# Performance work log

Measured on AMD Instinct MI355X. Metric: run time of the kernel, lower is better.

## Reference

```python
import jax, jax.numpy as jnp
import numpy as np

WH = WW = 7          # window size
N_TOK = WH * WW      # 49 tokens per window
HEADS = 8
HEAD_DIM = 32
DIM = HEADS * HEAD_DIM  # 256
NW = 64              # windows per image (56x56 / 7x7)
BW = 64 * NW         # batch_images * windows = 4096


def _rel_pos_index(wh, ww):
    # Swin-style relative position index, flattened to (N*N,)
    coords = np.stack(np.meshgrid(np.arange(wh), np.arange(ww), indexing='ij'))  # (2, wh, ww)
    coords = coords.reshape(2, -1)                                               # (2, N)
    rel = coords[:, :, None] - coords[:, None, :]                                # (2, N, N)
    rel = rel.transpose(1, 2, 0).astype(np.int64)                                # (N, N, 2)
    rel[:, :, 0] += wh - 1
    rel[:, :, 1] += ww - 1
    rel[:, :, 0] *= 2 * ww - 1
    return jnp.asarray(rel.sum(-1).reshape(-1))                                  # (N*N,)

_REL_IDX = _rel_pos_index(WH, WW)


def setup_inputs() -> dict:
    key = jax.random.key(0)
    ks = jax.random.split(key, 5)
    x = jax.random.normal(ks[0], (BW, N_TOK, DIM), dtype=jnp.float32)
    mask = jnp.zeros((1, NW, 1, N_TOK, N_TOK), dtype=jnp.float32)
    w_qkv = jax.random.normal(ks[1], (DIM, 3 * HEADS * HEAD_DIM), dtype=jnp.float32) * 0.02
    b_qkv = jnp.zeros((3 * HEADS * HEAD_DIM,), dtype=jnp.float32)
    rel_table = jax.random.normal(ks[2], ((2 * WH - 1) * (2 * WW - 1), HEADS), dtype=jnp.float32) * 0.02
    w_out = jax.random.normal(ks[3], (HEADS * HEAD_DIM, DIM), dtype=jnp.float32) * 0.02
    b_out = jnp.zeros((DIM,), dtype=jnp.float32)
    return {"x": x, "mask": mask, "w_qkv": w_qkv, "b_qkv": b_qkv,
            "rel_table": rel_table, "w_out": w_out, "b_out": b_out}


def reference(x, mask, w_qkv, b_qkv, rel_table, w_out, b_out):
    bw, n, d = x.shape
    # QKV projection then split per original Rearrange:
    # 'b n (qkv h hd) -> qkv b h n hd'
    qkv = (x @ w_qkv + b_qkv).reshape(bw, n, 3, HEADS, HEAD_DIM)
    qkv = qkv.transpose(2, 0, 3, 1, 4)  # (3, bw, h, n, hd)
    q, k, v = qkv[0], qkv[1], qkv[2]
    # NOTE: original computes einsum('bnid,bnjd->bnij', k, q): a[i,j] = k_i . q_j
    a = jnp.einsum('bhid,bhjd->bhij', k, q) / jnp.sqrt(jnp.asarray(HEAD_DIM, x.dtype))
    # relative position bias: table gather then '(i j) h -> h i j'
    bias = rel_table[_REL_IDX].reshape(n, n, HEADS).transpose(2, 0, 1)  # (h, n, n)
    a = a + bias
    # mask add: '(b nW) h i j -> b nW h i j', + mask, back
    nw = mask.shape[1]
    a = a.reshape(bw // nw, nw, HEADS, n, n) + mask
    a = a.reshape(bw, HEADS, n, n)
    a = jax.nn.softmax(a, axis=-1)
    y = jnp.einsum('bhij,bhjd->bhid', a, v)        # (bw, h, n, hd)
    y = y.transpose(0, 2, 1, 3).reshape(bw, n, HEADS * HEAD_DIM)
    return y @ w_out + b_out
```

## Files before the change

### kernel.cpp

```cpp
#include <hip/hip_runtime.h>

typedef __attribute__((ext_vector_type(8))) short short8;
typedef __attribute__((ext_vector_type(4))) float f32x4;
typedef unsigned short u16;

#define NTOK 49
#define NBLK 4096
#define LOG2E 1.4426950408889634f

#define XF  0
#define QKP 16384
#define VTF 49152
#define MKF 65536
#define POOLN 73728

#define WS_WQT 0
#define WS_WOT 393216
#define WS_BIAS 524288
#define WS_MKG 655360

__device__ __forceinline__ u16 f2bf(float f) {
  unsigned u = __float_as_uint(f);
  return (u16)((u + 0x7fffu + ((u >> 16) & 1u)) >> 16);
}
__device__ __forceinline__ unsigned packbf(float a, float b) {
  unsigned r;
  asm("v_cvt_pk_bf16_f32 %0, %1, %2" : "=v"(r) : "v"(a), "v"(b));
  return r;
}

__device__ __forceinline__ short8 asm_frag(unsigned c0p0, unsigned c0p1,
                                           unsigned c1p0, unsigned c1p1,
                                           int srcA, int srcB, bool cSel) {
  unsigned a0 = (unsigned)__shfl((int)c0p0, srcA);
  unsigned b0 = (unsigned)__shfl((int)c1p0, srcA);
  unsigned a1 = (unsigned)__shfl((int)c0p1, srcA);
  unsigned b1 = (unsigned)__shfl((int)c1p1, srcA);
  unsigned a2 = (unsigned)__shfl((int)c0p0, srcB);
  unsigned b2 = (unsigned)__shfl((int)c1p0, srcB);
  unsigned a3 = (unsigned)__shfl((int)c0p1, srcB);
  unsigned b3 = (unsigned)__shfl((int)c1p1, srcB);
  union { unsigned u[4]; short8 s8; } r;
  r.u[0] = cSel ? b0 : a0;
  r.u[1] = cSel ? b1 : a1;
  r.u[2] = cSel ? b2 : a2;
  r.u[3] = cSel ? b3 : a3;
  return r.s8;
}

__global__ void prep_kernel(const float* __restrict__ w_qkv,
                            const float* __restrict__ w_out,
                            const float* __restrict__ rel,
                            const float* __restrict__ mask,
                            u16* __restrict__ wqTf,
                            u16* __restrict__ woTf,
                            float* __restrict__ biasf,
                            float* __restrict__ mkg) {
  const int stride = gridDim.x * blockDim.x;
  const int gid = blockIdx.x * blockDim.x + threadIdx.x;
  for (int e = gid; e < 48 * 8 * 64 * 8; e += stride) {
    int eL = e & 7, ln = (e >> 3) & 63, ks = (e >> 9) & 7, ctg = e >> 12;
    int k = ks * 32 + (ln >> 4) * 8 + eL;
    int c = ctg * 16 + (ln & 15);
    wqTf[e] = f2bf(w_qkv[k * 768 + c]);
  }
  for (int e = gid; e < 16 * 8 * 64 * 8; e += stride) {
    int eL = e & 7, ln = (e >> 3) & 63, ks = (e >> 9) & 7, ctg = e >> 12;
    int k = ks * 32 + (ln >> 4) * 8 + eL;
    int c = ctg * 16 + (ln & 15);
    woTf[e] = f2bf(w_out[k * 256 + c]);
  }
  for (int e = gid; e < 8 * 16 * 64 * 4; e += stride) {
    int rg = e & 3, ln = (e >> 2) & 63, t = (e >> 8) & 15, hh = e >> 12;
    int i = (t >> 2) * 16 + (ln & 15);
    int j = (t & 3) * 16 + (ln >> 4) * 4 + rg;
    float v;
    if (j >= NTOK) v = -1e30f;
    else if (i >= NTOK) v = 0.f;
    else {
      int dh = i / 7 - j / 7 + 6;
      int dw = i % 7 - j % 7 + 6;
      v = rel[(dh * 13 + dw) * 8 + hh];
    }
    biasf[e] = v * LOG2E;
  }
  for (int e = gid; e < 64 * 16 * 64 * 4; e += stride) {
    int rg = e & 3, ln = (e >> 2) & 63, t = (e >> 8) & 15, wdw = e >> 12;
    int i = (t >> 2) * 16 + (ln & 15);
    int j = (t & 3) * 16 + (ln >> 4) * 4 + rg;
    mkg[e] = (i < NTOK && j < NTOK) ? mask[wdw * (NTOK * NTOK) + i * NTOK + j] * LOG2E : 0.f;
  }
}

__global__ void __launch_bounds__(1024, 4) winattn_mfma(
    const float* __restrict__ x,
    const float* __restrict__ b_qkv,
    const float* __restrict__ b_out,
    const u16* __restrict__ wqTf,
    const u16* __restrict__ woTf,
    const float* __restrict__ biasf,
    const float* __restrict__ mkg,
    float* __restrict__ out)
{
  __shared__ u16 pool[POOLN];
  const int b = blockIdx.x, tid = threadIdx.x;
  const int lane = tid & 63, lo = lane & 15, hi = lane >> 4;
  const int w = tid >> 6;
  const int h = w & 7;
  const int it0 = (w >> 3) * 2;
  const f32x4 zf = {0.f, 0.f, 0.f, 0.f};
  float* mkf = (float*)(pool + MKF);

  {
    const float4* xg = (const float4*)(x + (size_t)b * (NTOK * 256));
    for (int e = tid; e < 49 * 64; e += 1024) {
      float4 v = xg[e];
      int r = e >> 6, c4 = (e & 63) << 2;
      int addr = (((r >> 4) * 8 + (c4 >> 5)) * 64 + ((c4 >> 3) & 3) * 16 + (r & 15)) * 8 + (c4 & 7);
      *(uint2*)&pool[XF + addr] = make_uint2(packbf(v.x, v.y), packbf(v.z, v.w));
    }
    if (tid < 15 * 64) {
      int e = tid;
      int r = 49 + (e >> 6), c4 = (e & 63) << 2;
      int addr = (((r >> 4) * 8 + (c4 >> 5)) * 64 + ((c4 >> 3) & 3) * 16 + (r & 15)) * 8 + (c4 & 7);
      *(uint2*)&pool[XF + addr] = make_uint2(0u, 0u);
    }
    const float4* mg = (const float4*)(mkg + (size_t)(b & 63) * 4096);
    for (int e = tid; e < 1024; e += 1024) {
      *(float4*)&mkf[e * 4] = mg[e];
    }
  }
  __syncthreads();

  {
    const int ctq0 = 2 * w, ctq1 = 2 * w + 1, ctv = 32 + w;
    f32x4 acc[3][4];
    #pragma unroll
    for (int ct = 0; ct < 3; ++ct)
      #pragma unroll
      for (int rt = 0; rt < 4; ++rt) acc[ct][rt] = zf;
    #pragma unroll
    for (int ks = 0; ks < 8; ++ks) {
      short8 bx[4];
      #pragma unroll
      for (int rt = 0; rt < 4; ++rt)
        bx[rt] = *(const short8*)&pool[XF + ((rt * 8 + ks) * 64 + lane) * 8];
      short8 af0 = *(const short8*)&wqTf[((size_t)(ctq0 * 8 + ks) * 64 + lane) * 8];
      short8 af1 = *(const short8*)&wqTf[((size_t)(ctq1 * 8 + ks) * 64 + lane) * 8];
      short8 afv = *(const short8*)&wqTf[((size_t)(ctv * 8 + ks) * 64 + lane) * 8];
      #pragma unroll
      for (int rt = 0; rt < 4; ++rt) {
        acc[0][rt] = __builtin_amdgcn_mfma_f32_16x16x32_bf16(af0, bx[rt], acc[0][rt], 0, 0, 0);
        acc[1][rt] = __builtin_amdgcn_mfma_f32_16x16x32_bf16(af1, bx[rt], acc[1][rt], 0, 0, 0);
        acc[2][rt] = __builtin_amdgcn_mfma_f32_16x16x32_bf16(bx[rt], afv, acc[2][rt], 0, 0, 0);
      }
    }
    const int qkbase = QKP + (w & 7) * 4096 + ((w >= 8) ? 2048 : 0);
    #pragma unroll
    for (int ct = 0; ct < 2; ++ct) {
      const int ctg = 2 * w + ct;
      f32x4 bias = *(const f32x4*)(b_qkv + ctg * 16 + hi * 4);
      #pragma unroll
      for (int rt = 0; rt < 4; ++rt) {
        f32x4 v = acc[ct][rt] + bias;
        int hi2 = ct * 2 + (hi >> 1);
        int eb = (hi & 1) * 4;
        *(uint2*)&pool[qkbase + (rt * 64 + hi2 * 16 + lo) * 8 + eb] =
            make_uint2(packbf(v[0], v[1]), packbf(v[2], v[3]));
      }
    }
    {
      const int vhead = w >> 1, dblk = w & 1;
      const float bv = b_qkv[ctv * 16 + lo];
      #pragma unroll
      for (int rt = 0; rt < 4; ++rt) {
        f32x4 v = acc[2][rt];
        float v0 = v[0] + bv, v1 = v[1] + bv, v2 = v[2] + bv, v3 = v[3] + bv;
        int f = dblk * 2 + (rt >> 1);
        int hiR = (rt & 1) * 2 + (hi >> 1);
        int eb = (hi & 1) * 4;
        *(uint2*)&pool[VTF + (f * 8 + vhead) * 512 + (hiR * 16 + lo) * 8 + eb] =
            make_uint2(packbf(v0, v1), packbf(v2, v3));
      }
    }
  }
  __syncthreads();

  float rs0 = 0.f, rs1 = 0.f;
  unsigned pkp[4][2][2];
  {
    const float SC = 0.17677669529663687f * LOG2E;
    short8 ka0 = *(const short8*)&pool[QKP + h * 4096 + 2048 + ((it0 + 0) * 64 + lane) * 8];
    short8 ka1 = *(const short8*)&pool[QKP + h * 4096 + 2048 + ((it0 + 1) * 64 + lane) * 8];
    const float* bh = biasf + h * 4096;
    #pragma unroll
    for (int jt = 0; jt < 4; ++jt) {
      short8 qa = *(const short8*)&pool[QKP + h * 4096 + (jt * 64 + lane) * 8];
      f32x4 s0 = __builtin_amdgcn_mfma_f32_16x16x32_bf16(qa, ka0, zf, 0, 0, 0);
      f32x4 s1 = __builtin_amdgcn_mfma_f32_16x16x32_bf16(qa, ka1, zf, 0, 0, 0);
      {
        const int t = (it0 + 0) * 4 + jt;
        f32x4 bm = *(const f32x4*)&bh[(t * 64 + lane) * 4];
        f32x4 mm = *(const f32x4*)&mkf[(t * 64 + lane) * 4];
        float p0 = exp2f(fmaf(s0[0], SC, bm[0] + mm[0]));
        float p1 = exp2f(fmaf(s0[1], SC, bm[1] + mm[1]));
        float p2 = exp2f(fmaf(s0[2], SC, bm[2] + mm[2]));
        float p3 = exp2f(fmaf(s0[3], SC, bm[3] + mm[3]));
        rs0 += (p0 + p1) + (p2 + p3);
        pkp[jt][0][0] = packbf(p0, p1);
        pkp[jt][0][1] = packbf(p2, p3);
      }
      {
        const int t = (it0 + 1) * 4 + jt;
        f32x4 bm = *(const f32x4*)&bh[(t * 64 + lane) * 4];
        f32x4 mm = *(const f32x4*)&mkf[(t * 64 + lane) * 4];
        float p0 = exp2f(fmaf(s1[0], SC, bm[0] + mm[0]));
        float p1 = exp2f(fmaf(s1[1], SC, bm[1] + mm[1]));
        float p2 = exp2f(fmaf(s1[2], SC, bm[2] + mm[2]));
        float p3 = exp2f(fmaf(s1[3], SC, bm[3] + mm[3]));
        rs1 += (p0 + p1) + (p2 + p3);
        pkp[jt][1][0] = packbf(p0, p1);
        pkp[jt][1][1] = packbf(p2, p3);
      }
    }
  }
  float inv0, inv1;
  {
    float r2 = rs0 + __shfl_xor(rs0, 16);
    inv0 = 1.f / (r2 + __shfl_xor(r2, 32));
    float r3 = rs1 + __shfl_xor(rs1, 16);
    inv1 = 1.f / (r3 + __shfl_xor(r3, 32));
  }

  {
    const int srcA = lo + 32 * (hi & 1);
    const int srcB = srcA + 16;
    const bool cSel = (hi & 2) != 0;
    short8 va[2][2];
    #pragma unroll
    for (int dblk = 0; dblk < 2; ++dblk)
      #pragma unroll
      for (int k2 = 0; k2 < 2; ++k2)
        va[dblk][k2] = *(const short8*)&pool[VTF + ((dblk * 2 + k2) * 8 + h) * 512 + lane * 8];
    f32x4 ya[2][2];
    ya[0][0] = zf; ya[0][1] = zf; ya[1][0] = zf; ya[1][1] = zf;
    #pragma unroll
    for (int itL = 0; itL < 2; ++itL)
      #pragma unroll
      for (int k2 = 0; k2 < 2; ++k2) {
        short8 pb = asm_frag(pkp[2 * k2][itL][0], pkp[2 * k2][itL][1],
                             pkp[2 * k2 + 1][itL][0], pkp[2 * k2 + 1][itL][1], srcA, srcB, cSel);
        ya[0][itL] = __builtin_amdgcn_mfma_f32_16x16x32_bf16(va[0][k2], pb, ya[0][itL], 0, 0, 0);
        ya[1][itL] = __builtin_amdgcn_mfma_f32_16x16x32_bf16(va[1][k2], pb, ya[1][itL], 0, 0, 0);
      }
    #pragma unroll
    for (int itL = 0; itL < 2; ++itL) {
      const float iv = itL ? inv1 : inv0;
      #pragma unroll
      for (int dblk = 0; dblk < 2; ++dblk) {
        f32x4 yy = ya[dblk][itL];
        int hi2 = dblk * 2 + (hi >> 1);
        int eb = (hi & 1) * 4;
        *(uint2*)&pool[XF + (((it0 + itL) * 8 + h) * 64 + hi2 * 16 + lo) * 8 + eb] =
            make_uint2(packbf(yy[0] * iv, yy[1] * iv), packbf(yy[2] * iv, yy[3] * iv));
      }
    }
  }
  __syncthreads();

  {
    f32x4 pacc[4];
    pacc[0] = zf; pacc[1] = zf; pacc[2] = zf; pacc[3] = zf;
    #pragma unroll
    for (int ks = 0; ks < 8; ++ks) {
      short8 wf = *(const short8*)&woTf[((size_t)(w * 8 + ks) * 64 + lane) * 8];
      #pragma unroll
      for (int rt = 0; rt < 4; ++rt) {
        short8 yb = *(const short8*)&pool[XF + ((rt * 8 + ks) * 64 + lane) * 8];
        pacc[rt] = __builtin_amdgcn_mfma_f32_16x16x32_bf16(wf, yb, pacc[rt], 0, 0, 0);
      }
    }
    float* og = out + (size_t)b * (NTOK * 256);
    const int cb = w * 16 + hi * 4;
    f32x4 bb = *(const f32x4*)(b_out + cb);
    #pragma unroll
    for (int rt = 0; rt < 4; ++rt) {
      const int r = rt * 16 + lo;
      if (r < NTOK) {
        f32x4 vv = pacc[rt] + bb;
        *(f32x4*)(og + (size_t)r * 256 + cb) = vv;
      }
    }
  }
}

extern "C" void kernel_launch(void* const* d_in, const int* in_sizes, int n_in,
                              void* d_out, int out_size, void* d_ws, size_t ws_size,
                              hipStream_t stream) {
  const float *x = nullptr, *mask = nullptr, *w_qkv = nullptr, *b_qkv = nullptr,
              *rel_t = nullptr, *w_out = nullptr, *b_out = nullptr;
  for (int i = 0; i < n_in; ++i) {
    const float* p = (const float*)d_in[i];
    switch (in_sizes[i]) {
      case 4096 * 49 * 256: x = p; break;
      case 64 * 49 * 49:    mask = p; break;
      case 256 * 768:       w_qkv = p; break;
      case 768:             b_qkv = p; break;
      case 169 * 8:         rel_t = p; break;
      case 256 * 256:       w_out = p; break;
      case 256:             b_out = p; break;
    }
  }
  char* wsb = (char*)d_ws;
  u16* wqTf    = (u16*)(wsb + WS_WQT);
  u16* woTf    = (u16*)(wsb + WS_WOT);
  float* biasf = (float*)(wsb + WS_BIAS);
  float* mkg   = (float*)(wsb + WS_MKG);

  hipLaunchKernelGGL(prep_kernel, dim3(1024), dim3(256), 0, stream,
                     w_qkv, w_out, rel_t, mask, wqTf, woTf, biasf, mkg);
  hipLaunchKernelGGL(winattn_mfma, dim3(NBLK), dim3(1024), 0, stream,
                     x, b_qkv, b_out, wqTf, woTf, biasf, mkg, (float*)d_out);
}
```

Before: 301.7 us.

## Fold softmax scale into Q weights and precombine bias+mask table

Pre-scales the Q columns of the QKV weight and bias by the softmax scale times log2e, which removes a multiply from the score path. A new prep kernel builds a combined per-window, per-head bias+mask table (8 MB) in the workspace, so the main kernel reads one global table instead of staging the mask in shared memory. This shrinks LDS use and removes the mask load and the sync work that went with it. The trade is a larger global read footprint per block and an extra prep launch, with a fallback to the old path when the workspace is too small.

```diff
diff --git a/kernel.cpp b/kernel.cpp
--- a/kernel.cpp
+++ b/kernel.cpp
@@ -11,13 +11,15 @@
 #define XF  0
 #define QKP 16384
 #define VTF 49152
-#define MKF 65536
-#define POOLN 73728
+#define POOLN 65536
 
 #define WS_WQT 0
 #define WS_WOT 393216
-#define WS_BIAS 524288
-#define WS_MKG 655360
+#define WS_BQS 524288
+#define WS_BIAS 528384
+#define WS_MKG 659456
+#define WS_CMB 1708032
+#define WS_NEED (WS_CMB + 8388608)
 
 __device__ __forceinline__ u16 f2bf(float f) {
   unsigned u = __float_as_uint(f);
@@ -52,17 +54,22 @@
                             const float* __restrict__ w_out,
                             const float* __restrict__ rel,
                             const float* __restrict__ mask,
+                            const float* __restrict__ b_qkv,
                             u16* __restrict__ wqTf,
                             u16* __restrict__ woTf,
+                            float* __restrict__ bqs,
                             float* __restrict__ biasf,
                             float* __restrict__ mkg) {
+  const float SCQ = 0.17677669529663687f * LOG2E;
   const int stride = gridDim.x * blockDim.x;
   const int gid = blockIdx.x * blockDim.x + threadIdx.x;
   for (int e = gid; e < 48 * 8 * 64 * 8; e += stride) {
     int eL = e & 7, ln = (e >> 3) & 63, ks = (e >> 9) & 7, ctg = e >> 12;
     int k = ks * 32 + (ln >> 4) * 8 + eL;
     int c = ctg * 16 + (ln & 15);
-    wqTf[e] = f2bf(w_qkv[k * 768 + c]);
+    float wv = w_qkv[k * 768 + c];
+    if (ctg < 16) wv *= SCQ;
+    wqTf[e] = f2bf(wv);
   }
   for (int e = gid; e < 16 * 8 * 64 * 8; e += stride) {
     int eL = e & 7, ln = (e >> 3) & 63, ks = (e >> 9) & 7, ctg = e >> 12;
@@ -70,6 +77,8 @@
     int c = ctg * 16 + (ln & 15);
     woTf[e] = f2bf(w_out[k * 256 + c]);
   }
+  for (int e = gid; e < 768; e += stride)
+    bqs[e] = b_qkv[e] * (e < 256 ? SCQ : 1.f);
   for (int e = gid; e < 8 * 16 * 64 * 4; e += stride) {
     int rg = e & 3, ln = (e >> 2) & 63, t = (e >> 8) & 15, hh = e >> 12;
     int i = (t >> 2) * 16 + (ln & 15);
@@ -92,14 +101,25 @@
   }
 }
 
+__global__ void prep2_kernel(const float* __restrict__ biasf,
+                             const float* __restrict__ mkg,
+                             float* __restrict__ cmb) {
+  const int stride = gridDim.x * blockDim.x;
+  for (int e = blockIdx.x * blockDim.x + threadIdx.x; e < 64 * 8 * 4096; e += stride) {
+    int x = e & 4095, hh = (e >> 12) & 7, wdw = e >> 15;
+    cmb[e] = biasf[hh * 4096 + x] + mkg[wdw * 4096 + x];
+  }
+}
+
 __global__ void __launch_bounds__(1024, 4) winattn_mfma(
     const float* __restrict__ x,
-    const float* __restrict__ b_qkv,
+    const float* __restrict__ bqs,
     const float* __restrict__ b_out,
     const u16* __restrict__ wqTf,
     const u16* __restrict__ woTf,
     const float* __restrict__ biasf,
     const float* __restrict__ mkg,
+    const float* __restrict__ cmb,
     float* __restrict__ out)
 {
   __shared__ u16 pool[POOLN];
@@ -109,7 +129,6 @@
   const int h = w & 7;
   const int it0 = (w >> 3) * 2;
   const f32x4 zf = {0.f, 0.f, 0.f, 0.f};
-  float* mkf = (float*)(pool + MKF);
 
   {
     const float4* xg = (const float4*)(x + (size_t)b * (NTOK * 256));
@@ -125,10 +144,6 @@
       int addr = (((r >> 4) * 8 + (c4 >> 5)) * 64 + ((c4 >> 3) & 3) * 16 + (r & 15)) * 8 + (c4 & 7);
       *(uint2*)&pool[XF + addr] = make_uint2(0u, 0u);
     }
-    const float4* mg = (const float4*)(mkg + (size_t)(b & 63) * 4096);
-    for (int e = tid; e < 1024; e += 1024) {
-      *(float4*)&mkf[e * 4] = mg[e];
-    }
   }
   __syncthreads();
 
@@ -159,7 +174,7 @@
     #pragma unroll
     for (int ct = 0; ct < 2; ++ct) {
       const int ctg = 2 * w + ct;
-      f32x4 bias = *(const f32x4*)(b_qkv + ctg * 16 + hi * 4);
+      f32x4 bias = *(const f32x4*)(bqs + ctg * 16 + hi * 4);
       #pragma unroll
       for (int rt = 0; rt < 4; ++rt) {
         f32x4 v = acc[ct][rt] + bias;
@@ -171,7 +186,7 @@
     }
     {
       const int vhead = w >> 1, dblk = w & 1;
-      const float bv = b_qkv[ctv * 16 + lo];
+      const float bv = bqs[ctv * 16 + lo];
       #pragma unroll
       for (int rt = 0; rt < 4; ++rt) {
         f32x4 v = acc[2][rt];
@@ -189,10 +204,16 @@
   float rs0 = 0.f, rs1 = 0.f;
   unsigned pkp[4][2][2];
   {
-    const float SC = 0.17677669529663687f * LOG2E;
     short8 ka0 = *(const short8*)&pool[QKP + h * 4096 + 2048 + ((it0 + 0) * 64 + lane) * 8];
     short8 ka1 = *(const short8*)&pool[QKP + h * 4096 + 2048 + ((it0 + 1) * 64 + lane) * 8];
-    const float* bh = biasf + h * 4096;
+    const float* cb;
+    const float* mb = nullptr;
+    if (cmb) {
+      cb = cmb + (((size_t)(b & 63) * 8 + h) << 12);
+    } else {
+      cb = biasf + h * 4096;
+      mb = mkg + (size_t)(b & 63) * 4096;
+    }
     #pragma unroll
     for (int jt = 0; jt < 4; ++jt) {
       short8 qa = *(const short8*)&pool[QKP + h * 4096 + (jt * 64 + lane) * 8];
@@ -200,24 +221,30 @@
       f32x4 s1 = __builtin_amdgcn_mfma_f32_16x16x32_bf16(qa, ka1, zf, 0, 0, 0);
       {
         const int t = (it0 + 0) * 4 + jt;
-        f32x4 bm = *(const f32x4*)&bh[(t * 64 + lane) * 4];
-        f32x4 mm = *(const f32x4*)&mkf[(t * 64 + lane) * 4];
-        float p0 = exp2f(fmaf(s0[0], SC, bm[0] + mm[0]));
-        float p1 = exp2f(fmaf(s0[1], SC, bm[1] + mm[1]));
-        float p2 = exp2f(fmaf(s0[2], SC, bm[2] + mm[2]));
-        float p3 = exp2f(fmaf(s0[3], SC, bm[3] + mm[3]));
+        f32x4 c4 = *(const f32x4*)&cb[(t * 64 + lane) * 4];
+        if (mb) {
+          f32x4 m4 = *(const f32x4*)&mb[(t * 64 + lane) * 4];
+          c4[0] += m4[0]; c4[1] += m4[1]; c4[2] += m4[2]; c4[3] += m4[3];
+        }
+        float p0 = exp2f(s0[0] + c4[0]);
+        float p1 = exp2f(s0[1] + c4[1]);
+        float p2 = exp2f(s0[2] + c4[2]);
+        float p3 = exp2f(s0[3] + c4[3]);
         rs0 += (p0 + p1) + (p2 + p3);
         pkp[jt][0][0] = packbf(p0, p1);
         pkp[jt][0][1] = packbf(p2, p3);
       }
       {
         const int t = (it0 + 1) * 4 + jt;
-        f32x4 bm = *(const f32x4*)&bh[(t * 64 + lane) * 4];
-        f32x4 mm = *(const f32x4*)&mkf[(t * 64 + lane) * 4];
-        float p0 = exp2f(fmaf(s1[0], SC, bm[0] + mm[0]));
-        float p1 = exp2f(fmaf(s1[1], SC, bm[1] + mm[1]));
-        float p2 = exp2f(fmaf(s1[2], SC, bm[2] + mm[2]));
-        float p3 = exp2f(fmaf(s1[3], SC, bm[3] + mm[3]));
+        f32x4 c4 = *(const f32x4*)&cb[(t * 64 + lane) * 4];
+        if (mb) {
+          f32x4 m4 = *(const f32x4*)&mb[(t * 64 + lane) * 4];
+          c4[0] += m4[0]; c4[1] += m4[1]; c4[2] += m4[2]; c4[3] += m4[3];
+        }
+        float p0 = exp2f(s1[0] + c4[0]);
+        float p1 = exp2f(s1[1] + c4[1]);
+        float p2 = exp2f(s1[2] + c4[2]);
+        float p3 = exp2f(s1[3] + c4[3]);
         rs1 += (p0 + p1) + (p2 + p3);
         pkp[jt][1][0] = packbf(p0, p1);
         pkp[jt][1][1] = packbf(p2, p3);
@@ -281,14 +308,14 @@
       }
     }
     float* og = out + (size_t)b * (NTOK * 256);
-    const int cb = w * 16 + hi * 4;
-    f32x4 bb = *(const f32x4*)(b_out + cb);
+    const int cb2 = w * 16 + hi * 4;
+    f32x4 bb = *(const f32x4*)(b_out + cb2);
     #pragma unroll
     for (int rt = 0; rt < 4; ++rt) {
       const int r = rt * 16 + lo;
       if (r < NTOK) {
         f32x4 vv = pacc[rt] + bb;
-        *(f32x4*)(og + (size_t)r * 256 + cb) = vv;
+        *(f32x4*)(og + (size_t)r * 256 + cb2) = vv;
       }
     }
   }
@@ -314,11 +341,18 @@
   char* wsb = (char*)d_ws;
   u16* wqTf    = (u16*)(wsb + WS_WQT);
   u16* woTf    = (u16*)(wsb + WS_WOT);
+  float* bqs   = (float*)(wsb + WS_BQS);
   float* biasf = (float*)(wsb + WS_BIAS);
   float* mkg   = (float*)(wsb + WS_MKG);
+  const bool fits = (ws_size >= (size_t)WS_NEED);
+  float* cmb   = fits ? (float*)(wsb + WS_CMB) : nullptr;
 
   hipLaunchKernelGGL(prep_kernel, dim3(1024), dim3(256), 0, stream,
-                     w_qkv, w_out, rel_t, mask, wqTf, woTf, biasf, mkg);
+                     w_qkv, w_out, rel_t, mask, b_qkv, wqTf, woTf, bqs, biasf, mkg);
+  if (fits) {
+    hipLaunchKernelGGL(prep2_kernel, dim3(2048), dim3(256), 0, stream,
+                       biasf, mkg, cmb);
+  }
   hipLaunchKernelGGL(winattn_mfma, dim3(NBLK), dim3(1024), 0, stream,
-                     x, b_qkv, b_out, wqTf, woTf, biasf, mkg, (float*)d_out);
-}
+                     x, bqs, b_out, wqTf, woTf, biasf, mkg, cmb, (float*)d_out);
+}
```

Measured after the change: 282.2 us, median of 3. -6.5%, faster.
